# Optimization experiments

Measured on AMD Instinct MI355X. Metric: run time of the kernel, lower is better.

The kernel has to match this reference:

```python
import jax, jax.numpy as jnp
import numpy as np

B, Q, K, C, H, DH, OUT = 32, 512, 512, 256, 8, 32, 256


def setup_inputs() -> dict:
    key = jax.random.key(0)
    ks = jax.random.split(key, 11)
    s = 1.0 / np.sqrt(C)
    return {
        "q_data": jax.random.normal(ks[0], (B, Q, C), jnp.float32),
        "m_data": jax.random.normal(ks[1], (B, K, C), jnp.float32),
        "bias": jax.random.normal(ks[2], (B, 1, Q, K), jnp.float32),
        "nonbatched_bias": jax.random.normal(ks[3], (H, Q, K), jnp.float32),
        "query_w": jax.random.normal(ks[4], (C, H, DH), jnp.float32) * s,
        "key_w": jax.random.normal(ks[5], (C, H, DH), jnp.float32) * s,
        "value_w": jax.random.normal(ks[6], (C, H, DH), jnp.float32) * s,
        "gating_w": jax.random.normal(ks[7], (C, H, DH), jnp.float32) * s,
        "gating_b": jax.random.normal(ks[8], (H, DH), jnp.float32),
        "output_w": jax.random.normal(ks[9], (H, DH, OUT), jnp.float32) * (1.0 / np.sqrt(H * DH)),
        "output_b": jax.random.normal(ks[10], (OUT,), jnp.float32),
    }


def reference(q_data, m_data, bias, nonbatched_bias, query_w, key_w, value_w,
              gating_w, gating_b, output_w, output_b):
    key_dim = query_w.shape[-1]  # per-head key dim
    q = jnp.einsum('bqa,ahc->bqhc', q_data, query_w) * key_dim ** (-0.5)
    k = jnp.einsum('bka,ahc->bkhc', m_data, key_w)
    v = jnp.einsum('bka,ahc->bkhc', m_data, value_w)
    logits = jnp.einsum('bqhc,bkhc->bhqk', q, k) + bias  # [B,H,Q,K]
    logits = logits + nonbatched_bias[None]  # broadcast over batch
    logits = jnp.clip(logits, -1e8, 1e8)
    weights = jax.nn.softmax(logits, axis=-1)
    weighted_avg = jnp.einsum('bhqk,bkhc->bqhc', weights, v)
    gate = jax.nn.sigmoid(jnp.einsum('bqc,chv->bqhv', q_data, gating_w) + gating_b)
    weighted_avg = weighted_avg * gate
    return jnp.einsum('bqhc,hco->bqo', weighted_avg, output_w) + output_b
```

## Files before the change

kernel.cpp:

```cpp
#include <hip/hip_runtime.h>

typedef unsigned short u16;
typedef __attribute__((ext_vector_type(8))) short bf16x8;
typedef __attribute__((ext_vector_type(4))) float f32x4;

union Pack8 { u16 h[8]; int4 v; };
union Pack4 { u16 h[4]; uint2 v; };

__device__ __forceinline__ f32x4 mfma16(bf16x8 a, bf16x8 b, f32x4 c) {
    return __builtin_amdgcn_mfma_f32_16x16x32_bf16(a, b, c, 0, 0, 0);
}

__device__ __forceinline__ float bf2f(u16 u) {
    unsigned int x = ((unsigned int)u) << 16;
    return __builtin_bit_cast(float, x);
}

__device__ __forceinline__ u16 f2bf(float f) {
    unsigned int u = __builtin_bit_cast(unsigned int, f);
    u += 0x7FFF + ((u >> 16) & 1);
    return (u16)(u >> 16);
}

__global__ __launch_bounds__(256) void prep_w(
    const float* __restrict__ qw, const float* __restrict__ kw,
    const float* __restrict__ vw, const float* __restrict__ gw,
    const float* __restrict__ ow,
    u16* __restrict__ wtq, u16* __restrict__ wtm, u16* __restrict__ wto)
{
    const int which = blockIdx.y;
    const float* s = which == 0 ? qw : which == 1 ? kw : which == 2 ? vw
                   : which == 3 ? gw : ow;
    int n = blockIdx.x;
    int c = threadIdx.x;
    u16 val = f2bf(s[c * 256 + n]);
    if (which == 0)      wtq[n * 256 + c] = val;
    else if (which == 3) wtq[(256 + n) * 256 + c] = val;
    else if (which == 1) wtm[n * 256 + c] = val;
    else if (which == 2) wtm[(256 + n) * 256 + c] = val;
    else                 wto[n * 256 + c] = val;
}

__global__ __launch_bounds__(256) void conv_x(
    const float* __restrict__ q, const float* __restrict__ m,
    u16* __restrict__ qbf, u16* __restrict__ mbf)
{
    const float* s = blockIdx.y ? m : q;
    u16* d = blockIdx.y ? mbf : qbf;
    size_t i = ((size_t)blockIdx.x * 256 + threadIdx.x) * 4;
    float4 v = *(const float4*)(&s[i]);
    Pack4 p;
    p.h[0] = f2bf(v.x); p.h[1] = f2bf(v.y);
    p.h[2] = f2bf(v.z); p.h[3] = f2bf(v.w);
    *(uint2*)(&d[i]) = p.v;
}

__global__ __launch_bounds__(256) void proj128(
    const u16* __restrict__ qbf, const u16* __restrict__ mbf,
    const u16* __restrict__ wtq, const u16* __restrict__ wtm,
    const float* __restrict__ gating_b,
    u16* __restrict__ qbuf, u16* __restrict__ kbuf,
    u16* __restrict__ vbuf, u16* __restrict__ gbuf)
{
    const int src = blockIdx.z;
    const u16* X = src ? mbf : qbf;
    const u16* W = src ? wtm : wtq;

    const int m0 = blockIdx.x * 128;
    const int n0 = blockIdx.y * 128;

    __shared__ __align__(16) u16 Xs[128][72];
    __shared__ __align__(16) u16 Ws[128][72];

    const int tid  = threadIdx.x;
    const int wave = tid >> 6;
    const int wm   = wave >> 1, wn = wave & 1;
    const int lane = tid & 63;
    const int l16  = lane & 15;
    const int quad = lane >> 4;

    const f32x4 kZero = {0.f, 0.f, 0.f, 0.f};
    f32x4 acc[4][4];
    #pragma unroll
    for (int i = 0; i < 4; ++i)
        #pragma unroll
        for (int j = 0; j < 4; ++j) acc[i][j] = kZero;

    const int r  = tid >> 1;
    const int cs = (tid & 1) * 32;

    for (int k0 = 0; k0 < 256; k0 += 64) {
        __syncthreads();
        #pragma unroll
        for (int i = 0; i < 4; ++i) {
            *(int4*)(&Xs[r][cs + i * 8]) = *(const int4*)(&X[(size_t)(m0 + r) * 256 + k0 + cs + i * 8]);
            *(int4*)(&Ws[r][cs + i * 8]) = *(const int4*)(&W[(size_t)(n0 + r) * 256 + k0 + cs + i * 8]);
        }
        __syncthreads();
        #pragma unroll
        for (int ks = 0; ks < 2; ++ks) {
            bf16x8 a[4], bb[4];
            #pragma unroll
            for (int mf = 0; mf < 4; ++mf)
                a[mf] = *(const bf16x8*)(&Xs[wm * 64 + mf * 16 + l16][ks * 32 + quad * 8]);
            #pragma unroll
            for (int nf = 0; nf < 4; ++nf)
                bb[nf] = *(const bf16x8*)(&Ws[wn * 64 + nf * 16 + l16][ks * 32 + quad * 8]);
            #pragma unroll
            for (int mf = 0; mf < 4; ++mf)
                #pragma unroll
                for (int nf = 0; nf < 4; ++nf)
                    acc[mf][nf] = mfma16(a[mf], bb[nf], acc[mf][nf]);
        }
    }

    const bool second = (n0 >= 256);
    #pragma unroll
    for (int nf = 0; nf < 4; ++nf) {
        const int ng = n0 + wn * 64 + nf * 16 + l16;
        const int nl = second ? (ng - 256) : ng;
        const int h = nl >> 5, c = nl & 31;
        #pragma unroll
        for (int mf = 0; mf < 4; ++mf) {
            #pragma unroll
            for (int rr = 0; rr < 4; ++rr) {
                const int m = m0 + wm * 64 + mf * 16 + quad * 4 + rr;
                const int b = m >> 9, qi = m & 511;
                float v = acc[mf][nf][rr];
                size_t hidx = (((size_t)(b * 8 + h) * 512 + qi) * 32 + c);
                if (src == 0) {
                    if (!second) {
                        qbuf[hidx] = f2bf(v * 0.17677669529663689f);
                    } else {
                        float g = 1.0f / (1.0f + __expf(-(v + gating_b[nl])));
                        gbuf[(size_t)m * 256 + nl] = f2bf(g);
                    }
                } else {
                    if (!second) kbuf[hidx] = f2bf(v);
                    else         vbuf[hidx] = f2bf(v);
                }
            }
        }
    }
}

__global__ __launch_bounds__(256) void attn_kernel(
    const u16* __restrict__ qbuf, const u16* __restrict__ kbuf,
    const u16* __restrict__ vbuf, const float* __restrict__ bias,
    const float* __restrict__ nb, const u16* __restrict__ gbuf,
    u16* __restrict__ waG)
{
    const int b = blockIdx.z, h = blockIdx.y, q0 = blockIdx.x * 64;
    const int tid  = threadIdx.x;
    const int wave = tid >> 6;
    const int lane = tid & 63;
    const int l16  = lane & 15;
    const int quad = lane >> 4;

    __shared__ __align__(16) u16  Ks[64][40];
    __shared__ __align__(16) u16  Vs[32][72];
    __shared__ __align__(16) u16  Ps[4][16][72];
    __shared__ __align__(16) float Bs[64][68];

    const int qrow_base = q0 + wave * 16;
    bf16x8 aQ = *(const bf16x8*)(&qbuf[((b * 8 + h) * 512 + qrow_base + l16) * 32 + quad * 8]);

    const f32x4 kZero = {0.f, 0.f, 0.f, 0.f};
    f32x4 oacc[2] = {kZero, kZero};
    float lsum[4] = {0.f, 0.f, 0.f, 0.f};

    const int krow = tid >> 2, kseg = tid & 3;
    const int bq = tid >> 2,  bsg = tid & 3;
    const u16* kbase = &kbuf[(size_t)(b * 8 + h) * 512 * 32];
    const u16* vbase = &vbuf[(size_t)(b * 8 + h) * 512 * 32];
    const float* biasb = &bias[(size_t)b * 512 * 512 + (size_t)q0 * 512];
    const float* nbb   = &nb[(size_t)h * 512 * 512 + (size_t)q0 * 512];

    for (int kt = 0; kt < 8; ++kt) {
        const int kk0 = kt * 64;
        __syncthreads();
        *(int4*)(&Ks[krow][kseg * 8]) = *(const int4*)(&kbase[(kk0 + krow) * 32 + kseg * 8]);
        {
            Pack8 pv;
            pv.v = *(const int4*)(&vbase[(kk0 + krow) * 32 + kseg * 8]);
            #pragma unroll
            for (int i = 0; i < 8; ++i) Vs[kseg * 8 + i][krow] = pv.h[i];
        }
        #pragma unroll
        for (int i = 0; i < 4; ++i) {
            const int cidx = bsg * 16 + i * 4;
            float4 bbv = *(const float4*)(&biasb[(size_t)bq * 512 + kk0 + cidx]);
            float4 nnv = *(const float4*)(&nbb[(size_t)bq * 512 + kk0 + cidx]);
            float4 sum = make_float4(bbv.x + nnv.x, bbv.y + nnv.y,
                                     bbv.z + nnv.z, bbv.w + nnv.w);
            *(float4*)(&Bs[bq][cidx]) = sum;
        }
        __syncthreads();

        #pragma unroll
        for (int kn = 0; kn < 4; ++kn) {
            bf16x8 bK = *(const bf16x8*)(&Ks[kn * 16 + l16][quad * 8]);
            f32x4 s = mfma16(aQ, bK, kZero);
            #pragma unroll
            for (int rr = 0; rr < 4; ++rr) {
                float ls = s[rr] + Bs[wave * 16 + quad * 4 + rr][kn * 16 + l16];
                float p = __expf(ls);
                Ps[wave][quad * 4 + rr][kn * 16 + l16] = f2bf(p);
                lsum[rr] += p;
            }
        }

        __asm__ __volatile__("" ::: "memory");

        #pragma unroll
        for (int ct = 0; ct < 2; ++ct) {
            #pragma unroll
            for (int ks = 0; ks < 2; ++ks) {
                bf16x8 aP = *(const bf16x8*)(&Ps[wave][l16][ks * 32 + quad * 8]);
                bf16x8 bV = *(const bf16x8*)(&Vs[ct * 16 + l16][ks * 32 + quad * 8]);
                oacc[ct] = mfma16(aP, bV, oacc[ct]);
            }
        }
    }

    float linv[4];
    #pragma unroll
    for (int rr = 0; rr < 4; ++rr) {
        float v = lsum[rr];
        #pragma unroll
        for (int off = 1; off < 16; off <<= 1)
            v += __shfl_xor(v, off, 64);
        linv[rr] = 1.0f / v;
    }
    #pragma unroll
    for (int ct = 0; ct < 2; ++ct) {
        #pragma unroll
        for (int rr = 0; rr < 4; ++rr) {
            int qrow = qrow_base + quad * 4 + rr;
            int c = ct * 16 + l16;
            float o = oacc[ct][rr] * linv[rr];
            size_t idx = ((size_t)(b * 512 + qrow)) * 256 + h * 32 + c;
            float g = bf2f(gbuf[idx]);
            waG[idx] = f2bf(o * g);
        }
    }
}

__global__ __launch_bounds__(256) void out_gemm128(
    const u16* __restrict__ waG, const u16* __restrict__ wto,
    const float* __restrict__ out_b, float* __restrict__ out)
{
    const int m0 = blockIdx.x * 128;
    const int n0 = blockIdx.y * 128;

    __shared__ __align__(16) u16 Xs[128][72];
    __shared__ __align__(16) u16 Ws[128][72];

    const int tid  = threadIdx.x;
    const int wave = tid >> 6;
    const int wm   = wave >> 1, wn = wave & 1;
    const int lane = tid & 63;
    const int l16  = lane & 15;
    const int quad = lane >> 4;

    const f32x4 kZero = {0.f, 0.f, 0.f, 0.f};
    f32x4 acc[4][4];
    #pragma unroll
    for (int i = 0; i < 4; ++i)
        #pragma unroll
        for (int j = 0; j < 4; ++j) acc[i][j] = kZero;

    const int r  = tid >> 1;
    const int cs = (tid & 1) * 32;

    for (int k0 = 0; k0 < 256; k0 += 64) {
        __syncthreads();
        #pragma unroll
        for (int i = 0; i < 4; ++i) {
            *(int4*)(&Xs[r][cs + i * 8]) = *(const int4*)(&waG[(size_t)(m0 + r) * 256 + k0 + cs + i * 8]);
            *(int4*)(&Ws[r][cs + i * 8]) = *(const int4*)(&wto[(size_t)(n0 + r) * 256 + k0 + cs + i * 8]);
        }
        __syncthreads();
        #pragma unroll
        for (int ks = 0; ks < 2; ++ks) {
            bf16x8 a[4], bb[4];
            #pragma unroll
            for (int mf = 0; mf < 4; ++mf)
                a[mf] = *(const bf16x8*)(&Xs[wm * 64 + mf * 16 + l16][ks * 32 + quad * 8]);
            #pragma unroll
            for (int nf = 0; nf < 4; ++nf)
                bb[nf] = *(const bf16x8*)(&Ws[wn * 64 + nf * 16 + l16][ks * 32 + quad * 8]);
            #pragma unroll
            for (int mf = 0; mf < 4; ++mf)
                #pragma unroll
                for (int nf = 0; nf < 4; ++nf)
                    acc[mf][nf] = mfma16(a[mf], bb[nf], acc[mf][nf]);
        }
    }

    #pragma unroll
    for (int nf = 0; nf < 4; ++nf) {
        const int n = n0 + wn * 64 + nf * 16 + l16;
        const float ob = out_b[n];
        #pragma unroll
        for (int mf = 0; mf < 4; ++mf) {
            #pragma unroll
            for (int rr = 0; rr < 4; ++rr) {
                const int m = m0 + wm * 64 + mf * 16 + quad * 4 + rr;
                out[(size_t)m * 256 + n] = acc[mf][nf][rr] + ob;
            }
        }
    }
}

extern "C" void kernel_launch(void* const* d_in, const int* in_sizes, int n_in,
                              void* d_out, int out_size, void* d_ws, size_t ws_size,
                              hipStream_t stream)
{
    const float* q_data = (const float*)d_in[0];
    const float* m_data = (const float*)d_in[1];
    const float* bias   = (const float*)d_in[2];
    const float* nb     = (const float*)d_in[3];
    const float* qw     = (const float*)d_in[4];
    const float* kw     = (const float*)d_in[5];
    const float* vw     = (const float*)d_in[6];
    const float* gw     = (const float*)d_in[7];
    const float* gb     = (const float*)d_in[8];
    const float* ow     = (const float*)d_in[9];
    const float* ob     = (const float*)d_in[10];

    char* ws = (char*)d_ws;
    u16* wtq  = (u16*)ws;
    u16* wtm  = wtq + 131072;
    u16* wto  = wtm + 131072;
    u16* qbf  = wto + 65536;
    u16* mbf  = qbf + 4194304;
    u16* qbuf = mbf + 4194304;
    u16* kbuf = qbuf + 4194304;
    u16* vbuf = kbuf + 4194304;
    u16* gbuf = vbuf + 4194304;
    u16* waG  = gbuf + 4194304;

    prep_w<<<dim3(256, 5), 256, 0, stream>>>(qw, kw, vw, gw, ow, wtq, wtm, wto);
    conv_x<<<dim3(4096, 2), 256, 0, stream>>>(q_data, m_data, qbf, mbf);
    proj128<<<dim3(128, 4, 2), 256, 0, stream>>>(qbf, mbf, wtq, wtm, gb,
                                                 qbuf, kbuf, vbuf, gbuf);
    attn_kernel<<<dim3(8, 8, 32), 256, 0, stream>>>(qbuf, kbuf, vbuf, bias, nb,
                                                    gbuf, waG);
    out_gemm128<<<dim3(128, 2), 256, 0, stream>>>(waG, wto, ob, (float*)d_out);
}
```

Before: 223.5 us.

## Fuse input bf16 conversion into projection, transpose V, restructure attention to register P

Drops the separate conv_x kernel: proj128 now reads fp32 inputs and converts them to bf16 while staging into shared memory. The weight-prep kernel becomes a tiled shared-memory transpose. V is written pre-transposed, [dh][k], through an LDS staging tile, so attention loads it with plain vector copies. Attention now puts bias plus nonbatched bias straight into the MFMA accumulator and computes S transposed so P stays in registers. This removes the Bs/Ps shared buffers, and the gated output is written with vectorized stores. Softmax still uses no max subtraction, and the extra exp and bf16 conversion work is traded for less LDS traffic.

```diff
diff --git a/kernel.cpp b/kernel.cpp
--- a/kernel.cpp
+++ b/kernel.cpp
@@ -1,11 +1,12 @@
 #include <hip/hip_runtime.h>
 
 typedef unsigned short u16;
+typedef __attribute__((ext_vector_type(4))) short short4v;
 typedef __attribute__((ext_vector_type(8))) short bf16x8;
 typedef __attribute__((ext_vector_type(4))) float f32x4;
 
-union Pack8 { u16 h[8]; int4 v; };
-union Pack4 { u16 h[4]; uint2 v; };
+union Pack8 { u16 h[8]; int4 v; bf16x8 b; };
+union Frag8 { bf16x8 v8; short4v h4[2]; };
 
 __device__ __forceinline__ f32x4 mfma16(bf16x8 a, bf16x8 b, f32x4 c) {
     return __builtin_amdgcn_mfma_f32_16x16x32_bf16(a, b, c, 0, 0, 0);
@@ -22,55 +23,61 @@
     return (u16)(u >> 16);
 }
 
-__global__ __launch_bounds__(256) void prep_w(
+__global__ __launch_bounds__(256) void prep_w2(
     const float* __restrict__ qw, const float* __restrict__ kw,
     const float* __restrict__ vw, const float* __restrict__ gw,
     const float* __restrict__ ow,
     u16* __restrict__ wtq, u16* __restrict__ wtm, u16* __restrict__ wto)
 {
-    const int which = blockIdx.y;
+    const int which = blockIdx.z;
     const float* s = which == 0 ? qw : which == 1 ? kw : which == 2 ? vw
                    : which == 3 ? gw : ow;
-    int n = blockIdx.x;
-    int c = threadIdx.x;
-    u16 val = f2bf(s[c * 256 + n]);
-    if (which == 0)      wtq[n * 256 + c] = val;
-    else if (which == 3) wtq[(256 + n) * 256 + c] = val;
-    else if (which == 1) wtm[n * 256 + c] = val;
-    else if (which == 2) wtm[(256 + n) * 256 + c] = val;
-    else                 wto[n * 256 + c] = val;
-}
-
-__global__ __launch_bounds__(256) void conv_x(
-    const float* __restrict__ q, const float* __restrict__ m,
-    u16* __restrict__ qbf, u16* __restrict__ mbf)
-{
-    const float* s = blockIdx.y ? m : q;
-    u16* d = blockIdx.y ? mbf : qbf;
-    size_t i = ((size_t)blockIdx.x * 256 + threadIdx.x) * 4;
-    float4 v = *(const float4*)(&s[i]);
-    Pack4 p;
-    p.h[0] = f2bf(v.x); p.h[1] = f2bf(v.y);
-    p.h[2] = f2bf(v.z); p.h[3] = f2bf(v.w);
-    *(uint2*)(&d[i]) = p.v;
+    u16* d; int roff;
+    if (which == 0)      { d = wtq; roff = 0; }
+    else if (which == 3) { d = wtq; roff = 256; }
+    else if (which == 1) { d = wtm; roff = 0; }
+    else if (which == 2) { d = wtm; roff = 256; }
+    else                 { d = wto; roff = 0; }
+
+    const int n0 = blockIdx.x * 64;
+    const int c0 = blockIdx.y * 64;
+
+    __shared__ float T[64][68];
+    const int rr = threadIdx.x >> 2;
+    const int sg = threadIdx.x & 3;
+    #pragma unroll
+    for (int j = 0; j < 4; ++j) {
+        float4 v = *(const float4*)(&s[(size_t)(c0 + rr) * 256 + n0 + sg * 16 + j * 4]);
+        *(float4*)(&T[rr][sg * 16 + j * 4]) = v;
+    }
+    __syncthreads();
+    #pragma unroll
+    for (int j = 0; j < 4; ++j) {
+        union { u16 h[4]; uint2 v; } p;
+        #pragma unroll
+        for (int e = 0; e < 4; ++e)
+            p.h[e] = f2bf(T[sg * 16 + j * 4 + e][rr]);
+        *(uint2*)(&d[(size_t)(roff + n0 + rr) * 256 + c0 + sg * 16 + j * 4]) = p.v;
+    }
 }
 
 __global__ __launch_bounds__(256) void proj128(
-    const u16* __restrict__ qbf, const u16* __restrict__ mbf,
+    const float* __restrict__ q_data, const float* __restrict__ m_data,
     const u16* __restrict__ wtq, const u16* __restrict__ wtm,
     const float* __restrict__ gating_b,
     u16* __restrict__ qbuf, u16* __restrict__ kbuf,
     u16* __restrict__ vbuf, u16* __restrict__ gbuf)
 {
     const int src = blockIdx.z;
-    const u16* X = src ? mbf : qbf;
+    const float* X = src ? m_data : q_data;
     const u16* W = src ? wtm : wtq;
 
     const int m0 = blockIdx.x * 128;
     const int n0 = blockIdx.y * 128;
 
-    __shared__ __align__(16) u16 Xs[128][72];
-    __shared__ __align__(16) u16 Ws[128][72];
+    __shared__ __align__(16) u16 SMEM[2][128][72];
+    #define Xs (SMEM[0])
+    #define Ws (SMEM[1])
 
     const int tid  = threadIdx.x;
     const int wave = tid >> 6;
@@ -93,7 +100,14 @@
         __syncthreads();
         #pragma unroll
         for (int i = 0; i < 4; ++i) {
-            *(int4*)(&Xs[r][cs + i * 8]) = *(const int4*)(&X[(size_t)(m0 + r) * 256 + k0 + cs + i * 8]);
+            const float4* xp = (const float4*)(&X[(size_t)(m0 + r) * 256 + k0 + cs + i * 8]);
+            float4 xa = xp[0], xb = xp[1];
+            Pack8 pk;
+            pk.h[0] = f2bf(xa.x); pk.h[1] = f2bf(xa.y);
+            pk.h[2] = f2bf(xa.z); pk.h[3] = f2bf(xa.w);
+            pk.h[4] = f2bf(xb.x); pk.h[5] = f2bf(xb.y);
+            pk.h[6] = f2bf(xb.z); pk.h[7] = f2bf(xb.w);
+            *(int4*)(&Xs[r][cs + i * 8]) = pk.v;
             *(int4*)(&Ws[r][cs + i * 8]) = *(const int4*)(&W[(size_t)(n0 + r) * 256 + k0 + cs + i * 8]);
         }
         __syncthreads();
@@ -115,6 +129,33 @@
     }
 
     const bool second = (n0 >= 256);
+    const int b = m0 >> 9, qi0 = m0 & 511;
+
+    if (src == 1 && second) {
+        __syncthreads();
+        u16* T = &SMEM[0][0][0];
+        #pragma unroll
+        for (int nf = 0; nf < 4; ++nf) {
+            const int nl_ = wn * 64 + nf * 16 + l16;
+            #pragma unroll
+            for (int mf = 0; mf < 4; ++mf)
+                #pragma unroll
+                for (int rr = 0; rr < 4; ++rr) {
+                    const int ml = wm * 64 + mf * 16 + quad * 4 + rr;
+                    T[nl_ * 136 + ml] = f2bf(acc[mf][nf][rr]);
+                }
+        }
+        __syncthreads();
+        const int row = tid >> 1, half = tid & 1;
+        const int nl = (n0 - 256) + row;
+        const int h = nl >> 5, c = nl & 31;
+        u16* dst = &vbuf[((size_t)(b * 8 + h) * 32 + c) * 512 + qi0 + half * 64];
+        #pragma unroll
+        for (int i = 0; i < 8; ++i)
+            *(int4*)(&dst[i * 8]) = *(const int4*)(&T[row * 136 + half * 64 + i * 8]);
+        return;
+    }
+
     #pragma unroll
     for (int nf = 0; nf < 4; ++nf) {
         const int ng = n0 + wn * 64 + nf * 16 + l16;
@@ -125,7 +166,7 @@
             #pragma unroll
             for (int rr = 0; rr < 4; ++rr) {
                 const int m = m0 + wm * 64 + mf * 16 + quad * 4 + rr;
-                const int b = m >> 9, qi = m & 511;
+                const int qi = m & 511;
                 float v = acc[mf][nf][rr];
                 size_t hidx = (((size_t)(b * 8 + h) * 512 + qi) * 32 + c);
                 if (src == 0) {
@@ -136,12 +177,13 @@
                         gbuf[(size_t)m * 256 + nl] = f2bf(g);
                     }
                 } else {
-                    if (!second) kbuf[hidx] = f2bf(v);
-                    else         vbuf[hidx] = f2bf(v);
+                    kbuf[hidx] = f2bf(v);
                 }
             }
         }
     }
+    #undef Xs
+    #undef Ws
 }
 
 __global__ __launch_bounds__(256) void attn_kernel(
@@ -157,93 +199,92 @@
     const int l16  = lane & 15;
     const int quad = lane >> 4;
 
-    __shared__ __align__(16) u16  Ks[64][40];
-    __shared__ __align__(16) u16  Vs[32][72];
-    __shared__ __align__(16) u16  Ps[4][16][72];
-    __shared__ __align__(16) float Bs[64][68];
+    __shared__ __align__(16) u16 Ks[64][40];
+    __shared__ __align__(16) u16 Vs[32][72];
+    __shared__ __align__(16) u16 Os[4][16][40];
 
     const int qrow_base = q0 + wave * 16;
     bf16x8 aQ = *(const bf16x8*)(&qbuf[((b * 8 + h) * 512 + qrow_base + l16) * 32 + quad * 8]);
 
     const f32x4 kZero = {0.f, 0.f, 0.f, 0.f};
     f32x4 oacc[2] = {kZero, kZero};
-    float lsum[4] = {0.f, 0.f, 0.f, 0.f};
+    float lsum = 0.f;
 
     const int krow = tid >> 2, kseg = tid & 3;
-    const int bq = tid >> 2,  bsg = tid & 3;
+    const int vr = tid >> 3,  vseg = tid & 7;
     const u16* kbase = &kbuf[(size_t)(b * 8 + h) * 512 * 32];
-    const u16* vbase = &vbuf[(size_t)(b * 8 + h) * 512 * 32];
-    const float* biasb = &bias[(size_t)b * 512 * 512 + (size_t)q0 * 512];
-    const float* nbb   = &nb[(size_t)h * 512 * 512 + (size_t)q0 * 512];
+    const u16* vbase = &vbuf[(size_t)(b * 8 + h) * 32 * 512];
+    const float* blp = &bias[((size_t)b * 512 + qrow_base + l16) * 512];
+    const float* nlp = &nb[((size_t)h * 512 + qrow_base + l16) * 512];
 
     for (int kt = 0; kt < 8; ++kt) {
         const int kk0 = kt * 64;
+        float4 bb[4], nn[4];
+        #pragma unroll
+        for (int kn = 0; kn < 4; ++kn) {
+            bb[kn] = *(const float4*)(&blp[kk0 + kn * 16 + quad * 4]);
+            nn[kn] = *(const float4*)(&nlp[kk0 + kn * 16 + quad * 4]);
+        }
         __syncthreads();
         *(int4*)(&Ks[krow][kseg * 8]) = *(const int4*)(&kbase[(kk0 + krow) * 32 + kseg * 8]);
-        {
-            Pack8 pv;
-            pv.v = *(const int4*)(&vbase[(kk0 + krow) * 32 + kseg * 8]);
-            #pragma unroll
-            for (int i = 0; i < 8; ++i) Vs[kseg * 8 + i][krow] = pv.h[i];
-        }
-        #pragma unroll
-        for (int i = 0; i < 4; ++i) {
-            const int cidx = bsg * 16 + i * 4;
-            float4 bbv = *(const float4*)(&biasb[(size_t)bq * 512 + kk0 + cidx]);
-            float4 nnv = *(const float4*)(&nbb[(size_t)bq * 512 + kk0 + cidx]);
-            float4 sum = make_float4(bbv.x + nnv.x, bbv.y + nnv.y,
-                                     bbv.z + nnv.z, bbv.w + nnv.w);
-            *(float4*)(&Bs[bq][cidx]) = sum;
-        }
-        __syncthreads();
-
+        *(int4*)(&Vs[vr][vseg * 8])   = *(const int4*)(&vbase[vr * 512 + kk0 + vseg * 8]);
+        __syncthreads();
+
+        float p[4][4];
         #pragma unroll
         for (int kn = 0; kn < 4; ++kn) {
-            bf16x8 bK = *(const bf16x8*)(&Ks[kn * 16 + l16][quad * 8]);
-            f32x4 s = mfma16(aQ, bK, kZero);
+            f32x4 cb = {bb[kn].x + nn[kn].x, bb[kn].y + nn[kn].y,
+                        bb[kn].z + nn[kn].z, bb[kn].w + nn[kn].w};
+            bf16x8 aK = *(const bf16x8*)(&Ks[kn * 16 + l16][quad * 8]);
+            f32x4 st = mfma16(aK, aQ, cb);
             #pragma unroll
             for (int rr = 0; rr < 4; ++rr) {
-                float ls = s[rr] + Bs[wave * 16 + quad * 4 + rr][kn * 16 + l16];
-                float p = __expf(ls);
-                Ps[wave][quad * 4 + rr][kn * 16 + l16] = f2bf(p);
-                lsum[rr] += p;
-            }
-        }
-
-        __asm__ __volatile__("" ::: "memory");
-
-        #pragma unroll
-        for (int ct = 0; ct < 2; ++ct) {
-            #pragma unroll
-            for (int ks = 0; ks < 2; ++ks) {
-                bf16x8 aP = *(const bf16x8*)(&Ps[wave][l16][ks * 32 + quad * 8]);
-                bf16x8 bV = *(const bf16x8*)(&Vs[ct * 16 + l16][ks * 32 + quad * 8]);
-                oacc[ct] = mfma16(aP, bV, oacc[ct]);
-            }
-        }
-    }
-
-    float linv[4];
-    #pragma unroll
-    for (int rr = 0; rr < 4; ++rr) {
-        float v = lsum[rr];
-        #pragma unroll
-        for (int off = 1; off < 16; off <<= 1)
-            v += __shfl_xor(v, off, 64);
-        linv[rr] = 1.0f / v;
-    }
-    #pragma unroll
-    for (int ct = 0; ct < 2; ++ct) {
-        #pragma unroll
-        for (int rr = 0; rr < 4; ++rr) {
-            int qrow = qrow_base + quad * 4 + rr;
-            int c = ct * 16 + l16;
-            float o = oacc[ct][rr] * linv[rr];
-            size_t idx = ((size_t)(b * 512 + qrow)) * 256 + h * 32 + c;
-            float g = bf2f(gbuf[idx]);
-            waG[idx] = f2bf(o * g);
-        }
-    }
+                float pv = __expf(st[rr]);
+                p[kn][rr] = pv;
+                lsum += pv;
+            }
+        }
+
+        #pragma unroll
+        for (int pr = 0; pr < 2; ++pr) {
+            Frag8 bP;
+            #pragma unroll
+            for (int rr = 0; rr < 4; ++rr) {
+                bP.h4[0][rr] = (short)f2bf(p[2 * pr][rr]);
+                bP.h4[1][rr] = (short)f2bf(p[2 * pr + 1][rr]);
+            }
+            #pragma unroll
+            for (int ct = 0; ct < 2; ++ct) {
+                Frag8 aV;
+                aV.h4[0] = *(const short4v*)(&Vs[ct * 16 + l16][pr * 32 + quad * 4]);
+                aV.h4[1] = *(const short4v*)(&Vs[ct * 16 + l16][pr * 32 + 16 + quad * 4]);
+                oacc[ct] = mfma16(aV.v8, bP.v8, oacc[ct]);
+            }
+        }
+    }
+
+    lsum += __shfl_xor(lsum, 16, 64);
+    lsum += __shfl_xor(lsum, 32, 64);
+    const float linv = 1.0f / lsum;
+
+    #pragma unroll
+    for (int ct = 0; ct < 2; ++ct)
+        #pragma unroll
+        for (int rr = 0; rr < 4; ++rr)
+            Os[wave][l16][ct * 16 + quad * 4 + rr] = f2bf(oacc[ct][rr] * linv);
+
+    __asm__ __volatile__("" ::: "memory");
+
+    const int orow = lane >> 2, osg = lane & 3;
+    Pack8 ov, gv;
+    ov.v = *(const int4*)(&Os[wave][orow][osg * 8]);
+    size_t gidx = ((size_t)(b * 512 + q0 + wave * 16 + orow)) * 256 + h * 32 + osg * 8;
+    gv.v = *(const int4*)(&gbuf[gidx]);
+    Pack8 outv;
+    #pragma unroll
+    for (int i = 0; i < 8; ++i)
+        outv.h[i] = f2bf(bf2f(ov.h[i]) * bf2f(gv.h[i]));
+    *(int4*)(&waG[gidx]) = outv.v;
 }
 
 __global__ __launch_bounds__(256) void out_gemm128(
@@ -333,17 +374,14 @@
     u16* wtq  = (u16*)ws;
     u16* wtm  = wtq + 131072;
     u16* wto  = wtm + 131072;
-    u16* qbf  = wto + 65536;
-    u16* mbf  = qbf + 4194304;
-    u16* qbuf = mbf + 4194304;
+    u16* qbuf = wto + 65536;
     u16* kbuf = qbuf + 4194304;
     u16* vbuf = kbuf + 4194304;
     u16* gbuf = vbuf + 4194304;
     u16* waG  = gbuf + 4194304;
 
-    prep_w<<<dim3(256, 5), 256, 0, stream>>>(qw, kw, vw, gw, ow, wtq, wtm, wto);
-    conv_x<<<dim3(4096, 2), 256, 0, stream>>>(q_data, m_data, qbf, mbf);
-    proj128<<<dim3(128, 4, 2), 256, 0, stream>>>(qbf, mbf, wtq, wtm, gb,
+    prep_w2<<<dim3(4, 4, 5), 256, 0, stream>>>(qw, kw, vw, gw, ow, wtq, wtm, wto);
+    proj128<<<dim3(128, 4, 2), 256, 0, stream>>>(q_data, m_data, wtq, wtm, gb,
                                                  qbuf, kbuf, vbuf, gbuf);
     attn_kernel<<<dim3(8, 8, 32), 256, 0, stream>>>(qbuf, kbuf, vbuf, bias, nb,
                                                     gbuf, waG);
```

Result: slower. 242.5 us (+8.5%).
